# Kernel optimization log

Hardware: AMD Instinct MI355X
Metric: run time of the kernel (lower is better)

Reference implementation:

```python
import jax, jax.numpy as jnp
import numpy as np

NUM_HEADS = 32
ROPE_THETA = 10000.0


def _apply_rope_neox(x, positions):
    # x: [B, S, H, D], positions: [B, S]
    D = x.shape[-1]
    inv_freq = 1.0 / (ROPE_THETA ** (jnp.arange(0, D, 2, dtype=jnp.float32) / D))  # [D/2]
    ang = positions.astype(jnp.float32)[..., None] * inv_freq  # [B, S, D/2]
    cos = jnp.cos(ang)[:, :, None, :]  # [B, S, 1, D/2]
    sin = jnp.sin(ang)[:, :, None, :]
    x1, x2 = x[..., : D // 2], x[..., D // 2 :]
    return jnp.concatenate([x1 * cos - x2 * sin, x2 * cos + x1 * sin], axis=-1)


def setup_inputs() -> dict:
    key = jax.random.key(0)
    ks = jax.random.split(key, 4)
    B, S, H = 2, 2048, 4096
    positions = jnp.broadcast_to(jnp.arange(S, dtype=jnp.int32), (B, S))
    hidden_states = jax.random.normal(ks[0], (B, S, H), dtype=jnp.float32)
    w_qkv = jax.random.normal(ks[1], (H, 3 * H), dtype=jnp.float32) * (H ** -0.5)
    b_qkv = jax.random.normal(ks[2], (3 * H,), dtype=jnp.float32) * 0.02
    w_proj = jax.random.normal(ks[3], (H, H), dtype=jnp.float32) * (H ** -0.5)
    return {"positions": positions, "hidden_states": hidden_states,
            "w_qkv": w_qkv, "b_qkv": b_qkv, "w_proj": w_proj}


def reference(positions, hidden_states, w_qkv, b_qkv, w_proj):
    B, S, H = hidden_states.shape
    nh = NUM_HEADS
    hd = H // nh
    scale = hd ** -0.5

    qkv = hidden_states @ w_qkv + b_qkv  # [B, S, 3H]
    q, k, v = jnp.split(qkv, 3, axis=-1)
    q = q.reshape(B, S, nh, hd)
    k = k.reshape(B, S, nh, hd)
    v = v.reshape(B, S, nh, hd)

    q = _apply_rope_neox(q, positions)
    k = _apply_rope_neox(k, positions)

    scores = jnp.einsum("bqhd,bkhd->bhqk", q, k) * scale  # [B, H, S, S]
    causal = jnp.tril(jnp.ones((S, S), dtype=bool))
    scores = jnp.where(causal, scores, jnp.finfo(scores.dtype).min)
    probs = jax.nn.softmax(scores, axis=-1)
    attn = jnp.einsum("bhqk,bkhd->bqhd", probs, v).reshape(B, S, H)

    return attn @ w_proj
```

## Files before the change

### kernel.cpp

```cpp
#include <hip/hip_runtime.h>

#define NHD 32
#define SS  2048
#define HH  4096
#define H3  12288
#define HD  128

typedef __attribute__((ext_vector_type(4))) float f32x4;
typedef __attribute__((ext_vector_type(8))) short short8;

#define GLOAD_LDS16(gptr, lptr)                                                        \
  __builtin_amdgcn_global_load_lds((const __attribute__((address_space(1))) void*)(gptr), \
                                   (__attribute__((address_space(3))) void*)(lptr), 16, 0, 0)

__device__ __forceinline__ ushort f2bf(float f) {
  union { float f; unsigned u; } v; v.f = f;
  unsigned r = (v.u + 0x7FFFu + ((v.u >> 16) & 1u)) >> 16;
  return (ushort)r;
}
__device__ __forceinline__ float bf2f(ushort u) {
  union { unsigned u; float f; } v; v.u = ((unsigned)u) << 16;
  return v.f;
}

__global__ __launch_bounds__(256) void cvt_f32_bf16(const float* __restrict__ in,
                                                    ushort* __restrict__ out) {
  size_t i = ((size_t)blockIdx.x * 256 + threadIdx.x) * 4;
  float4 v = *(const float4*)(in + i);
  ushort4 r; r.x = f2bf(v.x); r.y = f2bf(v.y); r.z = f2bf(v.z); r.w = f2bf(v.w);
  *(ushort4*)(out + i) = r;
}

__global__ __launch_bounds__(256) void transpose_cvt(const float* __restrict__ in,
                                                     ushort* __restrict__ out,
                                                     int rows, int cols) {
  __shared__ float tile[32][33];
  int c0 = blockIdx.x * 32, r0 = blockIdx.y * 32;
  int tx = threadIdx.x, ty = threadIdx.y;
  #pragma unroll
  for (int i = ty; i < 32; i += 8)
    tile[i][tx] = in[(size_t)(r0 + i) * cols + (c0 + tx)];
  __syncthreads();
  #pragma unroll
  for (int i = ty; i < 32; i += 8)
    out[(size_t)(c0 + i) * rows + (r0 + tx)] = f2bf(tile[tx][i]);
}

template<bool BIAS, bool OUTBF16>
__global__ __launch_bounds__(256) void gemm_bf16(const ushort* __restrict__ A,
                                                 const ushort* __restrict__ BT,
                                                 const float* __restrict__ bias,
                                                 void* __restrict__ Cv,
                                                 int N, int K) {
  __shared__ __align__(16) ushort As[128 * 64];
  __shared__ __align__(16) ushort Bs[128 * 64];
  int tid  = threadIdx.x;
  int wave = tid >> 6, lane = tid & 63;
  int g = lane >> 4, q = lane & 15;
  int m0 = blockIdx.y * 128, n0 = blockIdx.x * 128;
  int wr = (wave >> 1) * 64, wc = (wave & 1) * 64;
  f32x4 acc[4][4] = {};
  for (int k0 = 0; k0 < K; k0 += 64) {
    __syncthreads();
    #pragma unroll
    for (int r = 0; r < 4; ++r) {
      int gr  = wave * 64 + 256 * r + lane;
      int row = gr >> 3, col = (gr & 7) << 3;
      int ldsbase = (wave * 64 + 256 * r) * 8;
      GLOAD_LDS16(A  + (size_t)(m0 + row) * K + k0 + col, &As[ldsbase]);
      GLOAD_LDS16(BT + (size_t)(n0 + row) * K + k0 + col, &Bs[ldsbase]);
    }
    __syncthreads();
    #pragma unroll
    for (int kk = 0; kk < 64; kk += 32) {
      short8 af[4], bfr[4];
      #pragma unroll
      for (int m = 0; m < 4; ++m)
        af[m] = *(const short8*)(&As[(wr + m * 16 + q) * 64 + kk + 8 * g]);
      #pragma unroll
      for (int n = 0; n < 4; ++n)
        bfr[n] = *(const short8*)(&Bs[(wc + n * 16 + q) * 64 + kk + 8 * g]);
      #pragma unroll
      for (int m = 0; m < 4; ++m)
        #pragma unroll
        for (int n = 0; n < 4; ++n)
          acc[m][n] = __builtin_amdgcn_mfma_f32_16x16x32_bf16(af[m], bfr[n], acc[m][n], 0, 0, 0);
    }
  }
  #pragma unroll
  for (int m = 0; m < 4; ++m) {
    #pragma unroll
    for (int n = 0; n < 4; ++n) {
      int gcol = n0 + wc + n * 16 + q;
      float bv = 0.f;
      if (BIAS) bv = bias[gcol];
      #pragma unroll
      for (int r = 0; r < 4; ++r) {
        int grow = m0 + wr + m * 16 + g * 4 + r;
        float v = acc[m][n][r] + bv;
        if (OUTBF16) ((ushort*)Cv)[(size_t)grow * N + gcol] = f2bf(v);
        else         ((float*) Cv)[(size_t)grow * N + gcol] = v;
      }
    }
  }
}

__global__ __launch_bounds__(256) void rope_split(const ushort* __restrict__ qkv,
                                                  const int* __restrict__ positions,
                                                  ushort* __restrict__ qb,
                                                  ushort* __restrict__ kb,
                                                  ushort* __restrict__ vb) {
  int id = blockIdx.x * 256 + threadIdx.x;
  int d = id & 63;
  int h = (id >> 6) & 31;
  int t = id >> 11;
  int b = t >> 11, s = t & 2047;
  float pos = (float)positions[t];
  float ang = pos * __expf(-(float)d * 0.14391156831212787f);
  float sv, cv;
  sincosf(ang, &sv, &cv);
  size_t src = (size_t)t * H3 + h * 128 + d;
  float q1 = bf2f(qkv[src]),        q2 = bf2f(qkv[src + 64]);
  float k1 = bf2f(qkv[src + 4096]), k2 = bf2f(qkv[src + 4160]);
  size_t dst = ((size_t)(b * NHD + h) * SS + s) * HD + d;
  qb[dst]      = f2bf(q1 * cv - q2 * sv);
  qb[dst + 64] = f2bf(q2 * cv + q1 * sv);
  kb[dst]      = f2bf(k1 * cv - k2 * sv);
  kb[dst + 64] = f2bf(k2 * cv + k1 * sv);
  vb[dst]      = qkv[src + 8192];
  vb[dst + 64] = qkv[src + 8256];
}

__global__ __launch_bounds__(256) void attn_fwd(const ushort* __restrict__ qb,
                                                const ushort* __restrict__ kb,
                                                const ushort* __restrict__ vb,
                                                ushort* __restrict__ aout) {
  __shared__ __align__(16) ushort Ks[32 * 136];
  __shared__ __align__(16) ushort Vt[128 * 40];
  __shared__ __align__(16) ushort Pw[4 * 16 * 40];
  const float SCALE = 0.08838834764831845f;
  int tid = threadIdx.x, wave = tid >> 6, lane = tid & 63;
  int g = lane >> 4, q = lane & 15;
  int bh = blockIdx.y;
  int qb0 = blockIdx.x * 64;
  const ushort* Kh = kb + (size_t)bh * SS * HD;
  const ushort* Vh = vb + (size_t)bh * SS * HD;
  const ushort* Qh = qb + (size_t)bh * SS * HD;

  short8 qf[4];
  int qrow = qb0 + wave * 16 + q;
  #pragma unroll
  for (int c = 0; c < 4; ++c)
    qf[c] = *(const short8*)(Qh + (size_t)qrow * HD + c * 32 + 8 * g);

  f32x4 o[8] = {};
  float mrow[4] = {-1e30f, -1e30f, -1e30f, -1e30f};
  float lrow[4] = {0.f, 0.f, 0.f, 0.f};

  int nt = qb0 / 32 + 2;
  for (int kt = 0; kt < nt; ++kt) {
    int kv0 = kt * 32;
    __syncthreads();
    #pragma unroll
    for (int r = 0; r < 2; ++r) {
      int gr = tid + 256 * r;
      int row = gr >> 4, col = (gr & 15) << 3;
      *(uint4*)(&Ks[row * 136 + col]) =
          *(const uint4*)(Kh + (size_t)(kv0 + row) * HD + col);
    }
    #pragma unroll
    for (int r = 0; r < 2; ++r) {
      int gr = tid + 256 * r;
      int row = gr >> 4, col = (gr & 15) << 3;
      uint4 v = *(const uint4*)(Vh + (size_t)(kv0 + row) * HD + col);
      ushort* pv = (ushort*)&v;
      #pragma unroll
      for (int i = 0; i < 8; ++i) Vt[(col + i) * 40 + row] = pv[i];
    }
    __syncthreads();

    f32x4 sf[2] = {};
    #pragma unroll
    for (int c = 0; c < 4; ++c) {
      #pragma unroll
      for (int n = 0; n < 2; ++n) {
        short8 kf = *(const short8*)(&Ks[(n * 16 + q) * 136 + c * 32 + 8 * g]);
        sf[n] = __builtin_amdgcn_mfma_f32_16x16x32_bf16(qf[c], kf, sf[n], 0, 0, 0);
      }
    }

    float corr[4];
    #pragma unroll
    for (int r = 0; r < 4; ++r) {
      int grow = qb0 + wave * 16 + g * 4 + r;
      float s0 = sf[0][r] * SCALE;
      float s1 = sf[1][r] * SCALE;
      if (kv0 + q > grow)      s0 = -1e30f;
      if (kv0 + 16 + q > grow) s1 = -1e30f;
      float mx = fmaxf(s0, s1);
      #pragma unroll
      for (int off = 8; off; off >>= 1) mx = fmaxf(mx, __shfl_xor(mx, off));
      float mnew = fmaxf(mrow[r], mx);
      corr[r] = __expf(mrow[r] - mnew);
      mrow[r] = mnew;
      float p0 = __expf(s0 - mnew);
      float p1 = __expf(s1 - mnew);
      float rs = p0 + p1;
      #pragma unroll
      for (int off = 8; off; off >>= 1) rs += __shfl_xor(rs, off);
      lrow[r] = lrow[r] * corr[r] + rs;
      Pw[wave * 640 + (g * 4 + r) * 40 + q]      = f2bf(p0);
      Pw[wave * 640 + (g * 4 + r) * 40 + 16 + q] = f2bf(p1);
    }
    #pragma unroll
    for (int d0 = 0; d0 < 8; ++d0)
      #pragma unroll
      for (int r = 0; r < 4; ++r) o[d0][r] *= corr[r];

    short8 pf = *(const short8*)(&Pw[wave * 640 + q * 40 + 8 * g]);
    #pragma unroll
    for (int d0 = 0; d0 < 8; ++d0) {
      short8 vf = *(const short8*)(&Vt[(d0 * 16 + q) * 40 + 8 * g]);
      o[d0] = __builtin_amdgcn_mfma_f32_16x16x32_bf16(pf, vf, o[d0], 0, 0, 0);
    }
  }

  int b = bh >> 5, h = bh & 31;
  #pragma unroll
  for (int r = 0; r < 4; ++r) {
    float inv = 1.0f / lrow[r];
    int srow = qb0 + wave * 16 + g * 4 + r;
    size_t base = ((size_t)(b * SS + srow)) * HH + h * 128;
    #pragma unroll
    for (int d0 = 0; d0 < 8; ++d0)
      aout[base + d0 * 16 + q] = f2bf(o[d0][r] * inv);
  }
}

extern "C" void kernel_launch(void* const* d_in, const int* in_sizes, int n_in,
                              void* d_out, int out_size, void* d_ws, size_t ws_size,
                              hipStream_t stream) {
  const int*   positions = (const int*)  d_in[0];
  const float* hidden    = (const float*)d_in[1];
  const float* w_qkv     = (const float*)d_in[2];
  const float* b_qkv     = (const float*)d_in[3];
  const float* w_proj    = (const float*)d_in[4];
  float* out = (float*)d_out;

  char* ws = (char*)d_ws;
  ushort* hsb   = (ushort*)(ws);
  ushort* wqkvT = (ushort*)(ws + 0x02000000ULL);
  ushort* wpT   = (ushort*)(ws + 0x08000000ULL);
  ushort* qkvb  = (ushort*)(ws + 0x0A000000ULL);
  ushort* qbuf  = (ushort*)(ws + 0x10000000ULL);
  ushort* kbuf  = (ushort*)(ws + 0x12000000ULL);
  ushort* vbuf  = (ushort*)(ws + 0x14000000ULL);
  ushort* aout  = hsb;

  cvt_f32_bf16<<<16384, 256, 0, stream>>>(hidden, hsb);
  transpose_cvt<<<dim3(384, 128), dim3(32, 8), 0, stream>>>(w_qkv, wqkvT, HH, H3);
  transpose_cvt<<<dim3(128, 128), dim3(32, 8), 0, stream>>>(w_proj, wpT, HH, HH);

  gemm_bf16<true, true><<<dim3(96, 32), 256, 0, stream>>>(hsb, wqkvT, b_qkv, qkvb, H3, HH);

  rope_split<<<32768, 256, 0, stream>>>(qkvb, positions, qbuf, kbuf, vbuf);

  attn_fwd<<<dim3(32, 64), 256, 0, stream>>>(qbuf, kbuf, vbuf, aout);

  gemm_bf16<false, false><<<dim3(32, 32), 256, 0, stream>>>(aout, wpT, nullptr, out, HH, HH);
}
```

Measured before the change: 2.089 ms.

## Enlarge attention tiles, pre-transpose V, and load K/V via swizzled direct-to-LDS loads

```diff
diff --git a/kernel.cpp b/kernel.cpp
--- a/kernel.cpp
+++ b/kernel.cpp
@@ -44,6 +44,21 @@
   #pragma unroll
   for (int i = ty; i < 32; i += 8)
     out[(size_t)(c0 + i) * rows + (r0 + tx)] = f2bf(tile[tx][i]);
+}
+
+__global__ __launch_bounds__(256) void vtrans(const ushort* __restrict__ qkvb,
+                                              ushort* __restrict__ vt) {
+  __shared__ ushort tile[32][33];
+  int s0 = blockIdx.x * 32, d0 = blockIdx.y * 32, bh = blockIdx.z;
+  int b = bh >> 5, h = bh & 31;
+  int tx = threadIdx.x, ty = threadIdx.y;
+  #pragma unroll
+  for (int i = ty; i < 32; i += 8)
+    tile[i][tx] = qkvb[(size_t)(b * SS + s0 + i) * H3 + 8192 + h * 128 + d0 + tx];
+  __syncthreads();
+  #pragma unroll
+  for (int i = ty; i < 32; i += 8)
+    vt[((size_t)bh * HD + d0 + i) * SS + s0 + tx] = tile[tx][i];
 }
 
 template<bool BIAS, bool OUTBF16>
@@ -108,8 +123,7 @@
 __global__ __launch_bounds__(256) void rope_split(const ushort* __restrict__ qkv,
                                                   const int* __restrict__ positions,
                                                   ushort* __restrict__ qb,
-                                                  ushort* __restrict__ kb,
-                                                  ushort* __restrict__ vb) {
+                                                  ushort* __restrict__ kb) {
   int id = blockIdx.x * 256 + threadIdx.x;
   int d = id & 63;
   int h = (id >> 6) & 31;
@@ -127,113 +141,144 @@
   qb[dst + 64] = f2bf(q2 * cv + q1 * sv);
   kb[dst]      = f2bf(k1 * cv - k2 * sv);
   kb[dst + 64] = f2bf(k2 * cv + k1 * sv);
-  vb[dst]      = qkv[src + 8192];
-  vb[dst + 64] = qkv[src + 8256];
 }
 
 __global__ __launch_bounds__(256) void attn_fwd(const ushort* __restrict__ qb,
                                                 const ushort* __restrict__ kb,
-                                                const ushort* __restrict__ vb,
+                                                const ushort* __restrict__ vt,
                                                 ushort* __restrict__ aout) {
-  __shared__ __align__(16) ushort Ks[32 * 136];
-  __shared__ __align__(16) ushort Vt[128 * 40];
-  __shared__ __align__(16) ushort Pw[4 * 16 * 40];
+  __shared__ __align__(16) ushort Ks[64 * 128];
+  __shared__ __align__(16) ushort Vs[128 * 64];
+  __shared__ __align__(16) ushort Pw[4 * 32 * 68];
   const float SCALE = 0.08838834764831845f;
   int tid = threadIdx.x, wave = tid >> 6, lane = tid & 63;
   int g = lane >> 4, q = lane & 15;
+  int swk = (q & 7) << 4;
   int bh = blockIdx.y;
-  int qb0 = blockIdx.x * 64;
+  int qb0 = blockIdx.x * 128;
+  const ushort* Qh = qb + (size_t)bh * SS * HD;
   const ushort* Kh = kb + (size_t)bh * SS * HD;
-  const ushort* Vh = vb + (size_t)bh * SS * HD;
-  const ushort* Qh = qb + (size_t)bh * SS * HD;
-
-  short8 qf[4];
-  int qrow = qb0 + wave * 16 + q;
-  #pragma unroll
-  for (int c = 0; c < 4; ++c)
-    qf[c] = *(const short8*)(Qh + (size_t)qrow * HD + c * 32 + 8 * g);
-
-  f32x4 o[8] = {};
-  float mrow[4] = {-1e30f, -1e30f, -1e30f, -1e30f};
-  float lrow[4] = {0.f, 0.f, 0.f, 0.f};
-
-  int nt = qb0 / 32 + 2;
+  const ushort* Vh = vt + (size_t)bh * SS * HD;
+  ushort* Pm = &Pw[wave * 32 * 68];
+
+  short8 qf[2][4];
+  #pragma unroll
+  for (int m = 0; m < 2; ++m)
+    #pragma unroll
+    for (int c = 0; c < 4; ++c)
+      qf[m][c] = *(const short8*)(Qh + (size_t)(qb0 + wave * 32 + m * 16 + q) * HD + c * 32 + 8 * g);
+
+  f32x4 o[2][8] = {};
+  float mrow[2][4], lrow[2][4];
+  #pragma unroll
+  for (int m = 0; m < 2; ++m)
+    #pragma unroll
+    for (int r = 0; r < 4; ++r) { mrow[m][r] = -1e30f; lrow[m][r] = 0.f; }
+
+  int nt = (qb0 >> 6) + 2;
   for (int kt = 0; kt < nt; ++kt) {
-    int kv0 = kt * 32;
+    int kv0 = kt * 64;
     __syncthreads();
     #pragma unroll
-    for (int r = 0; r < 2; ++r) {
-      int gr = tid + 256 * r;
-      int row = gr >> 4, col = (gr & 15) << 3;
-      *(uint4*)(&Ks[row * 136 + col]) =
-          *(const uint4*)(Kh + (size_t)(kv0 + row) * HD + col);
-    }
-    #pragma unroll
-    for (int r = 0; r < 2; ++r) {
-      int gr = tid + 256 * r;
-      int row = gr >> 4, col = (gr & 15) << 3;
-      uint4 v = *(const uint4*)(Vh + (size_t)(kv0 + row) * HD + col);
-      ushort* pv = (ushort*)&v;
-      #pragma unroll
-      for (int i = 0; i < 8; ++i) Vt[(col + i) * 40 + row] = pv[i];
+    for (int r = 0; r < 4; ++r) {
+      int gi  = r * 256 + tid;
+      int row = gi >> 4, xb = (gi & 15) << 4;
+      int src = xb ^ ((row & 7) << 4);
+      GLOAD_LDS16(Kh + (size_t)(kv0 + row) * HD + (src >> 1),
+                  &Ks[(r * 256 + wave * 64) * 8]);
+    }
+    #pragma unroll
+    for (int r = 0; r < 4; ++r) {
+      int gi  = r * 256 + tid;
+      int row = gi >> 3, xb = (gi & 7) << 4;
+      int src = xb ^ ((row & 7) << 4);
+      GLOAD_LDS16(Vh + (size_t)row * SS + kv0 + (src >> 1),
+                  &Vs[(r * 256 + wave * 64) * 8]);
     }
     __syncthreads();
 
-    f32x4 sf[2] = {};
+    f32x4 sf[2][4] = {};
     #pragma unroll
     for (int c = 0; c < 4; ++c) {
       #pragma unroll
-      for (int n = 0; n < 2; ++n) {
-        short8 kf = *(const short8*)(&Ks[(n * 16 + q) * 136 + c * 32 + 8 * g]);
-        sf[n] = __builtin_amdgcn_mfma_f32_16x16x32_bf16(qf[c], kf, sf[n], 0, 0, 0);
+      for (int n = 0; n < 4; ++n) {
+        int row = n * 16 + q;
+        short8 kf = *(const short8*)(&Ks[row * 128 + (((c * 64 + 16 * g) ^ swk) >> 1)]);
+        #pragma unroll
+        for (int m = 0; m < 2; ++m)
+          sf[m][n] = __builtin_amdgcn_mfma_f32_16x16x32_bf16(qf[m][c], kf, sf[m][n], 0, 0, 0);
       }
     }
 
-    float corr[4];
+    bool masked = (kt >= nt - 2);
+    float corr[2][4];
+    #pragma unroll
+    for (int m = 0; m < 2; ++m) {
+      #pragma unroll
+      for (int r = 0; r < 4; ++r) {
+        int qrow = qb0 + wave * 32 + m * 16 + g * 4 + r;
+        float x[4];
+        #pragma unroll
+        for (int n = 0; n < 4; ++n) {
+          x[n] = sf[m][n][r] * SCALE;
+          if (masked && (kv0 + n * 16 + q > qrow)) x[n] = -1e30f;
+        }
+        float mx = fmaxf(fmaxf(x[0], x[1]), fmaxf(x[2], x[3]));
+        #pragma unroll
+        for (int off = 8; off; off >>= 1) mx = fmaxf(mx, __shfl_xor(mx, off));
+        float mnew = fmaxf(mrow[m][r], mx);
+        corr[m][r] = __expf(mrow[m][r] - mnew);
+        mrow[m][r] = mnew;
+        float rs = 0.f;
+        #pragma unroll
+        for (int n = 0; n < 4; ++n) {
+          float p = __expf(x[n] - mnew);
+          rs += p;
+          Pm[(m * 16 + g * 4 + r) * 68 + n * 16 + q] = f2bf(p);
+        }
+        #pragma unroll
+        for (int off = 8; off; off >>= 1) rs += __shfl_xor(rs, off);
+        lrow[m][r] = lrow[m][r] * corr[m][r] + rs;
+      }
+    }
+    #pragma unroll
+    for (int m = 0; m < 2; ++m)
+      #pragma unroll
+      for (int d0 = 0; d0 < 8; ++d0)
+        #pragma unroll
+        for (int r = 0; r < 4; ++r) o[m][d0][r] *= corr[m][r];
+
+    short8 pf[2][2];
+    #pragma unroll
+    for (int m = 0; m < 2; ++m)
+      #pragma unroll
+      for (int c2 = 0; c2 < 2; ++c2)
+        pf[m][c2] = *(const short8*)(&Pm[(m * 16 + q) * 68 + c2 * 32 + 8 * g]);
+    #pragma unroll
+    for (int d0 = 0; d0 < 8; ++d0) {
+      int vrow = d0 * 16 + q;
+      short8 vf0 = *(const short8*)(&Vs[vrow * 64 + (((16 * g) ^ swk) >> 1)]);
+      short8 vf1 = *(const short8*)(&Vs[vrow * 64 + (((64 + 16 * g) ^ swk) >> 1)]);
+      #pragma unroll
+      for (int m = 0; m < 2; ++m) {
+        o[m][d0] = __builtin_amdgcn_mfma_f32_16x16x32_bf16(pf[m][0], vf0, o[m][d0], 0, 0, 0);
+        o[m][d0] = __builtin_amdgcn_mfma_f32_16x16x32_bf16(pf[m][1], vf1, o[m][d0], 0, 0, 0);
+      }
+    }
+  }
+
+  int b = bh >> 5, h = bh & 31;
+  #pragma unroll
+  for (int m = 0; m < 2; ++m) {
     #pragma unroll
     for (int r = 0; r < 4; ++r) {
-      int grow = qb0 + wave * 16 + g * 4 + r;
-      float s0 = sf[0][r] * SCALE;
-      float s1 = sf[1][r] * SCALE;
-      if (kv0 + q > grow)      s0 = -1e30f;
-      if (kv0 + 16 + q > grow) s1 = -1e30f;
-      float mx = fmaxf(s0, s1);
-      #pragma unroll
-      for (int off = 8; off; off >>= 1) mx = fmaxf(mx, __shfl_xor(mx, off));
-      float mnew = fmaxf(mrow[r], mx);
-      corr[r] = __expf(mrow[r] - mnew);
-      mrow[r] = mnew;
-      float p0 = __expf(s0 - mnew);
-      float p1 = __expf(s1 - mnew);
-      float rs = p0 + p1;
-      #pragma unroll
-      for (int off = 8; off; off >>= 1) rs += __shfl_xor(rs, off);
-      lrow[r] = lrow[r] * corr[r] + rs;
-      Pw[wave * 640 + (g * 4 + r) * 40 + q]      = f2bf(p0);
-      Pw[wave * 640 + (g * 4 + r) * 40 + 16 + q] = f2bf(p1);
-    }
-    #pragma unroll
-    for (int d0 = 0; d0 < 8; ++d0)
-      #pragma unroll
-      for (int r = 0; r < 4; ++r) o[d0][r] *= corr[r];
-
-    short8 pf = *(const short8*)(&Pw[wave * 640 + q * 40 + 8 * g]);
-    #pragma unroll
-    for (int d0 = 0; d0 < 8; ++d0) {
-      short8 vf = *(const short8*)(&Vt[(d0 * 16 + q) * 40 + 8 * g]);
-      o[d0] = __builtin_amdgcn_mfma_f32_16x16x32_bf16(pf, vf, o[d0], 0, 0, 0);
-    }
-  }
-
-  int b = bh >> 5, h = bh & 31;
-  #pragma unroll
-  for (int r = 0; r < 4; ++r) {
-    float inv = 1.0f / lrow[r];
-    int srow = qb0 + wave * 16 + g * 4 + r;
-    size_t base = ((size_t)(b * SS + srow)) * HH + h * 128;
-    #pragma unroll
-    for (int d0 = 0; d0 < 8; ++d0)
-      aout[base + d0 * 16 + q] = f2bf(o[d0][r] * inv);
+      float inv = 1.0f / lrow[m][r];
+      int srow = qb0 + wave * 32 + m * 16 + g * 4 + r;
+      size_t base = ((size_t)(b * SS + srow)) * HH + h * 128;
+      #pragma unroll
+      for (int d0 = 0; d0 < 8; ++d0)
+        aout[base + d0 * 16 + q] = f2bf(o[m][d0][r] * inv);
+    }
   }
 }
 
@@ -254,7 +299,7 @@
   ushort* qkvb  = (ushort*)(ws + 0x0A000000ULL);
   ushort* qbuf  = (ushort*)(ws + 0x10000000ULL);
   ushort* kbuf  = (ushort*)(ws + 0x12000000ULL);
-  ushort* vbuf  = (ushort*)(ws + 0x14000000ULL);
+  ushort* vtb   = (ushort*)(ws + 0x14000000ULL);
   ushort* aout  = hsb;
 
   cvt_f32_bf16<<<16384, 256, 0, stream>>>(hidden, hsb);
@@ -263,9 +308,10 @@
 
   gemm_bf16<true, true><<<dim3(96, 32), 256, 0, stream>>>(hsb, wqkvT, b_qkv, qkvb, H3, HH);
 
-  rope_split<<<32768, 256, 0, stream>>>(qkvb, positions, qbuf, kbuf, vbuf);
-
-  attn_fwd<<<dim3(32, 64), 256, 0, stream>>>(qbuf, kbuf, vbuf, aout);
+  rope_split<<<32768, 256, 0, stream>>>(qkvb, positions, qbuf, kbuf);
+  vtrans<<<dim3(64, 4, 64), dim3(32, 8), 0, stream>>>(qkvb, vtb);
+
+  attn_fwd<<<dim3(16, 64), 256, 0, stream>>>(qbuf, kbuf, vtb, aout);
 
   gemm_bf16<false, false><<<dim3(32, 32), 256, 0, stream>>>(aout, wpT, nullptr, out, HH, HH);
 }
```

Result: faster. 1.744 ms (-16.5%).
